# Kernel optimization log

Measured on AMD Instinct MI355X. Metric: run time of the kernel, lower is better.

The kernel has to match this reference:

```python
import jax, jax.numpy as jnp
import numpy as np

BN_EPS = 1e-5

def _conv2d(x, w, b, stride, padding, groups=1):
    out = jax.lax.conv_general_dilated(
        x, w, (stride, stride), padding,
        feature_group_count=groups,
        dimension_numbers=('NCHW', 'OIHW', 'NCHW'))
    return out + b[None, :, None, None]

def _bn(x, g, be, m, v):
    # eval-mode BatchNorm2d
    scale = g / jnp.sqrt(v + BN_EPS)
    return (x - m[None, :, None, None]) * scale[None, :, None, None] + be[None, :, None, None]

def _gelu(x):
    return jax.nn.gelu(x, approximate=False)  # torch nn.GELU default = exact erf

def _forward(x, conv0_w, conv0_b, bn0_g, bn0_b, bn0_m, bn0_v,
             dw_w, dw_b, bn1_g, bn1_b, bn1_m, bn1_v,
             pw_w, pw_b, bn2_g, bn2_b, bn2_m, bn2_v,
             lstm_w, lstm_b, fc_w, fc_b):
    B = x.shape[0]
    nh = conv0_w.shape[0]
    # stem: 4x4 stride-4 conv + BN + GELU -> [B, nh, 8, L]
    y = _gelu(_bn(_conv2d(x, conv0_w, conv0_b, 4, 'VALID'),
                  bn0_g, bn0_b, bn0_m, bn0_v))
    D = dw_w.shape[0]
    for i in range(D):  # MicroBlocks: residual depthwise 3x3 then pointwise 1x1
        r = _gelu(_bn(_conv2d(y, dw_w[i][:, None], dw_b[i], 1, [(1, 1), (1, 1)], groups=nh),
                      bn1_g[i], bn1_b[i], bn1_m[i], bn1_v[i]))
        y = y + r
        y = _gelu(_bn(_conv2d(y, pw_w[i][:, :, None, None], pw_b[i], 1, 'VALID'),
                      bn2_g[i], bn2_b[i], bn2_m[i], bn2_v[i]))
    # ConvLSTM: channel dim nh is the time axis; state is [B, F=8, L]
    L = y.shape[3]
    F = lstm_w.shape[0] // 4
    seq = jnp.transpose(y, (1, 0, 2, 3))  # [nh, B, 8, L]
    h0 = jnp.zeros((B, F, L), y.dtype)

    def step(carry, xt):
        h, c = carry
        comb = jnp.concatenate([xt, h], axis=1)  # [B, 16, L]
        # kernel-size-1 Conv1d == per-position matmul
        A = jnp.einsum('oc,bcl->bol', lstm_w, comb) + lstm_b[None, :, None]
        ai, af, ao, ag = jnp.split(A, 4, axis=1)
        nc = jax.nn.sigmoid(af) * c + jax.nn.sigmoid(ai) * jnp.tanh(ag)
        nhd = jax.nn.sigmoid(ao) * jnp.tanh(nc)
        return (nhd, nc), nhd

    _, ys = jax.lax.scan(step, (h0, h0), seq)  # ys: [nh, B, 8, L]
    feat = jnp.transpose(ys, (1, 0, 2, 3)).reshape(B, nh * F, L)
    # adaptive_avg_pool1d to output size L (== input length) is identity;
    # dropout in eval mode is identity.
    logits = jnp.einsum('bcl,nc->bln', feat, fc_w) + fc_b  # [B, L, nclass]
    return logits

def setup_inputs():
    B, W, NH, D, NCLS, F = 32, 1024, 256, 4, 6625, 8
    key = jax.random.key(0)
    ks = jax.random.split(key, 24)
    n = lambda i, shape, s=0.05: jax.random.normal(ks[i], shape, jnp.float32) * s
    return {
        'x': jax.random.normal(ks[0], (B, 3, 32, W), jnp.float32),
        'conv0_w': n(1, (NH, 3, 4, 4)), 'conv0_b': n(2, (NH,)),
        'bn0_g': 1.0 + n(3, (NH,)), 'bn0_b': n(4, (NH,)),
        'bn0_m': n(5, (NH,)), 'bn0_v': 0.5 + jax.random.uniform(ks[6], (NH,), jnp.float32),
        'dw_w': n(7, (D, NH, 3, 3)), 'dw_b': n(8, (D, NH)),
        'bn1_g': 1.0 + n(9, (D, NH)), 'bn1_b': n(10, (D, NH)),
        'bn1_m': n(11, (D, NH)), 'bn1_v': 0.5 + jax.random.uniform(ks[12], (D, NH), jnp.float32),
        'pw_w': n(13, (D, NH, NH)), 'pw_b': n(14, (D, NH)),
        'bn2_g': 1.0 + n(15, (D, NH)), 'bn2_b': n(16, (D, NH)),
        'bn2_m': n(17, (D, NH)), 'bn2_v': 0.5 + jax.random.uniform(ks[18], (D, NH), jnp.float32),
        'lstm_w': n(19, (4 * F, 2 * F), 0.1), 'lstm_b': n(20, (4 * F,)),
        'fc_w': n(21, (NCLS, NH * F), 0.02), 'fc_b': n(22, (NCLS,)),
    }

def reference(x, conv0_w, conv0_b, bn0_g, bn0_b, bn0_m, bn0_v,
              dw_w, dw_b, bn1_g, bn1_b, bn1_m, bn1_v,
              pw_w, pw_b, bn2_g, bn2_b, bn2_m, bn2_v,
              lstm_w, lstm_b, fc_w, fc_b):
    return _forward(x, conv0_w, conv0_b, bn0_g, bn0_b, bn0_m, bn0_v,
                    dw_w, dw_b, bn1_g, bn1_b, bn1_m, bn1_v,
                    pw_w, pw_b, bn2_g, bn2_b, bn2_m, bn2_v,
                    lstm_w, lstm_b, fc_w, fc_b)
```

## Files before the change

### kernel.cpp

```cpp
#include <hip/hip_runtime.h>
#include <hip/hip_bf16.h>
#include <stdint.h>

#define BNEPS 1e-5f

typedef __bf16 bf16x8 __attribute__((ext_vector_type(8)));
typedef float f32x4 __attribute__((ext_vector_type(4)));

__device__ __forceinline__ float gelu_f(float x) {
    return 0.5f * x * (1.0f + erff(x * 0.70710678118654752440f));
}
__device__ __forceinline__ float sigmoid_f(float x) {
    return 1.0f / (1.0f + __expf(-x));
}
__device__ __forceinline__ float tanh_f(float x) {
    x = fminf(fmaxf(x, -15.0f), 15.0f);
    const float e = __expf(2.0f * x);
    return (e - 1.0f) / (e + 1.0f);
}
__device__ __forceinline__ void async16(const void* g, void* l) {
    __builtin_amdgcn_global_load_lds(
        (const __attribute__((address_space(1))) void*)g,
        (__attribute__((address_space(3))) void*)l,
        16, 0, 0);
}

__global__ __launch_bounds__(256)
void stem_kernel(const float* __restrict__ x, const float* __restrict__ w,
                 const float* __restrict__ cb,
                 const float* __restrict__ bg, const float* __restrict__ bb,
                 const float* __restrict__ bm, const float* __restrict__ bv,
                 float* __restrict__ y0)
{
    __shared__ float sw[64 * 48];
    const int ho = blockIdx.x, b = blockIdx.y, co0 = blockIdx.z * 64;
    const int wo = threadIdx.x;
    for (int i = threadIdx.x; i < 64 * 48; i += 256) sw[i] = w[co0 * 48 + i];
    float p[48];
    #pragma unroll
    for (int c = 0; c < 3; ++c)
        #pragma unroll
        for (int kh = 0; kh < 4; ++kh) {
            const float4 q = *reinterpret_cast<const float4*>(
                &x[((size_t)(b * 3 + c) * 32 + ho * 4 + kh) * 1024 + wo * 4]);
            p[c * 16 + kh * 4 + 0] = q.x;
            p[c * 16 + kh * 4 + 1] = q.y;
            p[c * 16 + kh * 4 + 2] = q.z;
            p[c * 16 + kh * 4 + 3] = q.w;
        }
    __syncthreads();
    for (int c2 = 0; c2 < 64; ++c2) {
        const int co = co0 + c2;
        const float* wp = &sw[c2 * 48];
        float a0 = 0.f, a1 = 0.f, a2 = 0.f, a3 = 0.f;
        #pragma unroll
        for (int i = 0; i < 12; ++i) {
            const float4 wq = *reinterpret_cast<const float4*>(&wp[i * 4]);
            a0 += wq.x * p[i * 4 + 0];
            a1 += wq.y * p[i * 4 + 1];
            a2 += wq.z * p[i * 4 + 2];
            a3 += wq.w * p[i * 4 + 3];
        }
        const float acc = (a0 + a1) + (a2 + a3) + cb[co];
        const float sc = bg[co] / sqrtf(bv[co] + BNEPS);
        const float val = (acc - bm[co]) * sc + bb[co];
        y0[((size_t)(b * 256 + co) * 8 + ho) * 256 + wo] = gelu_f(val);
    }
}

__global__ __launch_bounds__(256)
void dw_kernel(const float* __restrict__ y0, const float* __restrict__ dww,
               const float* __restrict__ dwb,
               const float* __restrict__ bg, const float* __restrict__ bb,
               const float* __restrict__ bm, const float* __restrict__ bv,
               __hip_bfloat16* __restrict__ y1)
{
    __shared__ float tile[8][258];
    const int c = blockIdx.x, b = blockIdx.y, t = threadIdx.x;
    const float* src = &y0[(size_t)(b * 256 + c) * 2048];
    #pragma unroll
    for (int r = 0; r < 8; ++r) tile[r][1 + t] = src[r * 256 + t];
    if (t < 8) { tile[t][0] = 0.f; tile[t][257] = 0.f; }
    float w9[9];
    #pragma unroll
    for (int i = 0; i < 9; ++i) w9[i] = dww[c * 9 + i];
    const float bias = dwb[c];
    const float sc = bg[c] / sqrtf(bv[c] + BNEPS);
    const float sb = bb[c] - bm[c] * sc;
    __syncthreads();
    __hip_bfloat16* dst = &y1[(size_t)(b * 256 + c) * 2048];
    #pragma unroll
    for (int r = 0; r < 8; ++r) {
        float acc = bias;
        #pragma unroll
        for (int kh = 0; kh < 3; ++kh) {
            const int rr = r + kh - 1;
            if (rr < 0 || rr > 7) continue;
            acc += w9[kh * 3 + 0] * tile[rr][t] + w9[kh * 3 + 1] * tile[rr][t + 1]
                 + w9[kh * 3 + 2] * tile[rr][t + 2];
        }
        const float val = gelu_f(acc * sc + sb);
        dst[r * 256 + t] = __float2bfloat16(tile[r][t + 1] + val);
    }
}

__global__ __launch_bounds__(256)
void tr_kernel(const __hip_bfloat16* __restrict__ y1, __hip_bfloat16* __restrict__ y1t)
{
    __shared__ __hip_bfloat16 tile[64][65];
    const int hw0 = blockIdx.x * 64, c0 = blockIdx.y * 64, b = blockIdx.z;
    const int tx = threadIdx.x & 63, ty = threadIdx.x >> 6;
    const __hip_bfloat16* src = &y1[((size_t)b * 256 + c0) * 2048 + hw0];
    #pragma unroll
    for (int r = ty; r < 64; r += 4) tile[r][tx] = src[(size_t)r * 2048 + tx];
    __syncthreads();
    __hip_bfloat16* dst = &y1t[((size_t)b * 2048 + hw0) * 256 + c0];
    #pragma unroll
    for (int r = ty; r < 64; r += 4) dst[(size_t)r * 256 + tx] = tile[tx][r];
}

template<int EPI>
__global__ __launch_bounds__(256)
void gemm_kernel(const __hip_bfloat16* __restrict__ A,
                 const __hip_bfloat16* __restrict__ Bt,
                 float* __restrict__ out, int K, int NT,
                 const float* __restrict__ q0, const float* __restrict__ q1,
                 const float* __restrict__ q2, const float* __restrict__ q3,
                 const float* __restrict__ q4)
{
    __shared__ __hip_bfloat16 sA[2][4096];
    __shared__ __hip_bfloat16 sB[2][4096];
    const int tid = threadIdx.x;
    const int wave = tid >> 6, lane = tid & 63;
    const int m0 = blockIdx.y * 128, n0 = blockIdx.x * 128;

    auto stage = [&](int buf, int kt) {
        const int k0 = kt << 5;
        #pragma unroll
        for (int r = 0; r < 2; ++r) {
            const int e = wave * 1024 + r * 512 + lane * 8;
            const int row = e >> 5, ko = e & 31;
            async16(&A[(size_t)(m0 + row) * K + k0 + ko], &sA[buf][wave * 1024 + r * 512]);
            async16(&Bt[(size_t)(n0 + row) * K + k0 + ko], &sB[buf][wave * 1024 + r * 512]);
        }
    };

    f32x4 acc[4][4];
    #pragma unroll
    for (int i = 0; i < 4; ++i)
        #pragma unroll
        for (int j = 0; j < 4; ++j) acc[i][j] = (f32x4){0.f, 0.f, 0.f, 0.f};

    stage(0, 0);
    const int wm = wave >> 1, wn = wave & 1;
    const int lrow = lane & 15, lgrp = lane >> 4;
    int cur = 0;
    for (int kt = 0; kt < NT; ++kt) {
        __syncthreads();
        if (kt + 1 < NT) stage(cur ^ 1, kt + 1);
        bf16x8 av[4], bw[4];
        #pragma unroll
        for (int i = 0; i < 4; ++i) {
            av[i] = *reinterpret_cast<const bf16x8*>(&sA[cur][(wm * 64 + i * 16 + lrow) * 32 + lgrp * 8]);
            bw[i] = *reinterpret_cast<const bf16x8*>(&sB[cur][(wn * 64 + i * 16 + lrow) * 32 + lgrp * 8]);
        }
        #pragma unroll
        for (int mi = 0; mi < 4; ++mi)
            #pragma unroll
            for (int ni = 0; ni < 4; ++ni)
                acc[mi][ni] = __builtin_amdgcn_mfma_f32_16x16x32_bf16(av[mi], bw[ni], acc[mi][ni], 0, 0, 0);
        cur ^= 1;
    }

    #pragma unroll
    for (int mi = 0; mi < 4; ++mi) {
        const int rowb = m0 + wm * 64 + mi * 16 + lgrp * 4;
        #pragma unroll
        for (int ni = 0; ni < 4; ++ni) {
            const int col = n0 + wn * 64 + ni * 16 + lrow;
            #pragma unroll
            for (int r = 0; r < 4; ++r) {
                const float v = acc[mi][ni][r];
                if (EPI == 0) {
                    const int co = rowb + r;
                    const float sc = q1[co] / sqrtf(q4[co] + BNEPS);
                    const float sb = q2[co] - q3[co] * sc;
                    const float val = gelu_f((v + q0[co]) * sc + sb);
                    const int b_ = col >> 11, hw = col & 2047;
                    out[((size_t)b_ * 256 + co) * 2048 + hw] = val;
                } else {
                    if (col < 6625)
                        out[(size_t)(rowb + r) * 6625 + col] = v + q0[col];
                }
            }
        }
    }
}

__global__ __launch_bounds__(256)
void lstm_kernel(const float* __restrict__ y, const float* __restrict__ lw,
                 const float* __restrict__ lb, __hip_bfloat16* __restrict__ Am)
{
    const int gid = blockIdx.x * 256 + threadIdx.x;
    const int f = gid & 7, pos = gid >> 3;
    const int l = pos & 255, b = pos >> 8;
    float W[4][16], bias[4];
    #pragma unroll
    for (int g = 0; g < 4; ++g) {
        #pragma unroll
        for (int j = 0; j < 16; ++j) W[g][j] = lw[(g * 8 + f) * 16 + j];
        bias[g] = lb[g * 8 + f];
    }
    float h = 0.f, c = 0.f;
    const float* xb = y + (size_t)b * 524288 + f * 256 + l;
    __hip_bfloat16* ob = Am + (size_t)pos * 2048 + f;
    float xn = xb[0];
    for (int t = 0; t < 256; ++t) {
        const float xt = xn;
        if (t < 255) xn = xb[(size_t)(t + 1) * 2048];
        float A0 = bias[0], A1 = bias[1], A2 = bias[2], A3 = bias[3];
        #pragma unroll
        for (int j = 0; j < 8; ++j) {
            const float xj = __shfl(xt, j, 8);
            const float hj = __shfl(h, j, 8);
            A0 += W[0][j] * xj + W[0][8 + j] * hj;
            A1 += W[1][j] * xj + W[1][8 + j] * hj;
            A2 += W[2][j] * xj + W[2][8 + j] * hj;
            A3 += W[3][j] * xj + W[3][8 + j] * hj;
        }
        c = sigmoid_f(A1) * c + sigmoid_f(A0) * tanh_f(A3);
        h = sigmoid_f(A2) * tanh_f(c);
        ob[t * 8] = __float2bfloat16(h);
    }
}

__global__ void cvt_pww_kernel(const float* __restrict__ w, __hip_bfloat16* __restrict__ o, int n)
{
    const int i = blockIdx.x * 256 + threadIdx.x;
    if (i < n) o[i] = __float2bfloat16(w[i]);
}
__global__ void cvt_fcw_kernel(const float* __restrict__ w, __hip_bfloat16* __restrict__ o)
{
    const size_t i = (size_t)blockIdx.x * 256 + threadIdx.x;
    const size_t nrow = i >> 11, k = i & 2047;
    o[i] = (nrow < 6625) ? __float2bfloat16(w[nrow * 2048 + k]) : __float2bfloat16(0.0f);
}

extern "C" void kernel_launch(void* const* d_in, const int* in_sizes, int n_in,
                              void* d_out, int out_size, void* d_ws, size_t ws_size,
                              hipStream_t stream)
{
    const float* x       = (const float*)d_in[0];
    const float* conv0_w = (const float*)d_in[1];
    const float* conv0_b = (const float*)d_in[2];
    const float* bn0_g   = (const float*)d_in[3];
    const float* bn0_b   = (const float*)d_in[4];
    const float* bn0_m   = (const float*)d_in[5];
    const float* bn0_v   = (const float*)d_in[6];
    const float* dw_w    = (const float*)d_in[7];
    const float* dw_b    = (const float*)d_in[8];
    const float* bn1_g   = (const float*)d_in[9];
    const float* bn1_b   = (const float*)d_in[10];
    const float* bn1_m   = (const float*)d_in[11];
    const float* bn1_v   = (const float*)d_in[12];
    const float* pw_w    = (const float*)d_in[13];
    const float* pw_b    = (const float*)d_in[14];
    const float* bn2_g   = (const float*)d_in[15];
    const float* bn2_b   = (const float*)d_in[16];
    const float* bn2_m   = (const float*)d_in[17];
    const float* bn2_v   = (const float*)d_in[18];
    const float* lstm_w  = (const float*)d_in[19];
    const float* lstm_b  = (const float*)d_in[20];
    const float* fc_w    = (const float*)d_in[21];
    const float* fc_b    = (const float*)d_in[22];

    char* ws = (char*)d_ws;
    float* y0            = (float*)(ws);
    __hip_bfloat16* y1   = (__hip_bfloat16*)(ws + 67108864);
    __hip_bfloat16* y1t  = (__hip_bfloat16*)(ws + 100663296);
    __hip_bfloat16* fcwb = (__hip_bfloat16*)(ws + 134217728);
    __hip_bfloat16* pwwb = (__hip_bfloat16*)(ws + 161480704);
    __hip_bfloat16* Am   = (__hip_bfloat16*)(ws + 67108864);

    stem_kernel<<<dim3(8, 32, 4), 256, 0, stream>>>(
        x, conv0_w, conv0_b, bn0_g, bn0_b, bn0_m, bn0_v, y0);
    cvt_pww_kernel<<<1024, 256, 0, stream>>>(pw_w, pwwb, 262144);
    cvt_fcw_kernel<<<53248, 256, 0, stream>>>(fc_w, fcwb);

    for (int i = 0; i < 4; ++i) {
        dw_kernel<<<dim3(256, 32), 256, 0, stream>>>(
            y0, dw_w + i * 2304, dw_b + i * 256,
            bn1_g + i * 256, bn1_b + i * 256, bn1_m + i * 256, bn1_v + i * 256, y1);
        tr_kernel<<<dim3(32, 4, 32), 256, 0, stream>>>(y1, y1t);
        gemm_kernel<0><<<dim3(512, 2), 256, 0, stream>>>(
            pwwb + i * 65536, y1t, y0, 256, 8,
            pw_b + i * 256, bn2_g + i * 256, bn2_b + i * 256, bn2_m + i * 256, bn2_v + i * 256);
    }

    lstm_kernel<<<256, 256, 0, stream>>>(y0, lstm_w, lstm_b, Am);

    gemm_kernel<1><<<dim3(52, 64), 256, 0, stream>>>(
        Am, fcwb, (float*)d_out, 2048, 64,
        fc_b, nullptr, nullptr, nullptr, nullptr);
}
```

Baseline: 767.6 us.

## Specialize FC GEMM with 256x256 tiles, triple buffering, LDS swizzle, block swizzle

After: 710.9 us. -7.4%, faster.

```diff
diff --git a/kernel.cpp b/kernel.cpp
--- a/kernel.cpp
+++ b/kernel.cpp
@@ -119,14 +119,13 @@
     for (int r = ty; r < 64; r += 4) dst[(size_t)r * 256 + tx] = tile[tx][r];
 }
 
-template<int EPI>
 __global__ __launch_bounds__(256)
-void gemm_kernel(const __hip_bfloat16* __restrict__ A,
-                 const __hip_bfloat16* __restrict__ Bt,
-                 float* __restrict__ out, int K, int NT,
-                 const float* __restrict__ q0, const float* __restrict__ q1,
-                 const float* __restrict__ q2, const float* __restrict__ q3,
-                 const float* __restrict__ q4)
+void gemm_pw_kernel(const __hip_bfloat16* __restrict__ A,
+                    const __hip_bfloat16* __restrict__ Bt,
+                    float* __restrict__ out, int K, int NT,
+                    const float* __restrict__ q0, const float* __restrict__ q1,
+                    const float* __restrict__ q2, const float* __restrict__ q3,
+                    const float* __restrict__ q4)
 {
     __shared__ __hip_bfloat16 sA[2][4096];
     __shared__ __hip_bfloat16 sB[2][4096];
@@ -181,17 +180,117 @@
             #pragma unroll
             for (int r = 0; r < 4; ++r) {
                 const float v = acc[mi][ni][r];
-                if (EPI == 0) {
-                    const int co = rowb + r;
-                    const float sc = q1[co] / sqrtf(q4[co] + BNEPS);
-                    const float sb = q2[co] - q3[co] * sc;
-                    const float val = gelu_f((v + q0[co]) * sc + sb);
-                    const int b_ = col >> 11, hw = col & 2047;
-                    out[((size_t)b_ * 256 + co) * 2048 + hw] = val;
-                } else {
-                    if (col < 6625)
-                        out[(size_t)(rowb + r) * 6625 + col] = v + q0[col];
-                }
+                const int co = rowb + r;
+                const float sc = q1[co] / sqrtf(q4[co] + BNEPS);
+                const float sb = q2[co] - q3[co] * sc;
+                const float val = gelu_f((v + q0[co]) * sc + sb);
+                const int b_ = col >> 11, hw = col & 2047;
+                out[((size_t)b_ * 256 + co) * 2048 + hw] = val;
+            }
+        }
+    }
+}
+
+__global__ __launch_bounds__(512, 2)
+void gemm_fc_kernel(const __hip_bfloat16* __restrict__ A,
+                    const __hip_bfloat16* __restrict__ Bt,
+                    const float* __restrict__ fcb,
+                    float* __restrict__ out)
+{
+    constexpr int K = 2048, NT = 64, NTILE = 26;
+    __shared__ __hip_bfloat16 smem[49152];
+    const int tid = threadIdx.x, wave = tid >> 6, lane = tid & 63;
+    const int wm = wave >> 2, wn = wave & 3;
+    const int r = lane & 15, g = lane >> 4;
+    const int swzk = (g ^ ((r >> 1) & 3)) * 8;
+
+    const int bid = blockIdx.x;
+    const int swz = (bid & 7) * 104 + (bid >> 3);
+    const int m0 = (swz / NTILE) * 256;
+    const int n0 = (swz % NTILE) * 256;
+
+    auto stageA = [&](int buf, int kt) {
+        #pragma unroll
+        for (int r2 = 0; r2 < 2; ++r2) {
+            const int e = wave * 128 + r2 * 64 + lane;
+            const int row = e >> 2, slot = e & 3;
+            const int kg = slot ^ ((row >> 1) & 3);
+            async16(&A[(size_t)(m0 + row) * K + kt * 32 + kg * 8],
+                    &smem[buf * 8192 + wave * 1024 + r2 * 512]);
+        }
+    };
+    auto stageB = [&](int buf, int kt) {
+        #pragma unroll
+        for (int r2 = 0; r2 < 2; ++r2) {
+            const int e = wave * 128 + r2 * 64 + lane;
+            const int row = e >> 2, slot = e & 3;
+            const int kg = slot ^ ((row >> 1) & 3);
+            async16(&Bt[(size_t)(n0 + row) * K + kt * 32 + kg * 8],
+                    &smem[24576 + buf * 8192 + wave * 1024 + r2 * 512]);
+        }
+    };
+
+    f32x4 acc[8][4];
+    #pragma unroll
+    for (int i = 0; i < 8; ++i)
+        #pragma unroll
+        for (int j = 0; j < 4; ++j) acc[i][j] = (f32x4){0.f, 0.f, 0.f, 0.f};
+
+    stageA(0, 0); stageB(0, 0);
+    stageA(1, 1); stageB(1, 1);
+
+    int bc = 0;
+    for (int kt = 0; kt < NT; ++kt) {
+        if (kt < NT - 1) asm volatile("s_waitcnt vmcnt(4)" ::: "memory");
+        else             asm volatile("s_waitcnt vmcnt(0)" ::: "memory");
+        asm volatile("s_barrier" ::: "memory");
+
+        const int bn = (bc + 2 >= 3) ? bc - 1 : bc + 2;
+        if (kt + 2 < NT) stageA(bn, kt + 2);
+
+        const __hip_bfloat16* pA = &smem[bc * 8192];
+        const __hip_bfloat16* pB = &smem[24576 + bc * 8192];
+        bf16x8 av[8];
+        #pragma unroll
+        for (int mi = 0; mi < 8; ++mi)
+            av[mi] = *reinterpret_cast<const bf16x8*>(&pA[(wm * 128 + mi * 16 + r) * 32 + swzk]);
+        bf16x8 b0 = *reinterpret_cast<const bf16x8*>(&pB[(wn * 64 + 0 * 16 + r) * 32 + swzk]);
+        bf16x8 b1 = *reinterpret_cast<const bf16x8*>(&pB[(wn * 64 + 1 * 16 + r) * 32 + swzk]);
+
+        __builtin_amdgcn_s_setprio(1);
+        #pragma unroll
+        for (int mi = 0; mi < 8; ++mi) {
+            acc[mi][0] = __builtin_amdgcn_mfma_f32_16x16x32_bf16(av[mi], b0, acc[mi][0], 0, 0, 0);
+            acc[mi][1] = __builtin_amdgcn_mfma_f32_16x16x32_bf16(av[mi], b1, acc[mi][1], 0, 0, 0);
+        }
+        __builtin_amdgcn_s_setprio(0);
+
+        if (kt + 2 < NT) stageB(bn, kt + 2);
+        bf16x8 b2 = *reinterpret_cast<const bf16x8*>(&pB[(wn * 64 + 2 * 16 + r) * 32 + swzk]);
+        bf16x8 b3 = *reinterpret_cast<const bf16x8*>(&pB[(wn * 64 + 3 * 16 + r) * 32 + swzk]);
+
+        __builtin_amdgcn_s_setprio(1);
+        #pragma unroll
+        for (int mi = 0; mi < 8; ++mi) {
+            acc[mi][2] = __builtin_amdgcn_mfma_f32_16x16x32_bf16(av[mi], b2, acc[mi][2], 0, 0, 0);
+            acc[mi][3] = __builtin_amdgcn_mfma_f32_16x16x32_bf16(av[mi], b3, acc[mi][3], 0, 0, 0);
+        }
+        __builtin_amdgcn_s_setprio(0);
+
+        bc = (bc == 2) ? 0 : bc + 1;
+    }
+
+    #pragma unroll
+    for (int mi = 0; mi < 8; ++mi) {
+        const int rowb = m0 + wm * 128 + mi * 16 + g * 4;
+        #pragma unroll
+        for (int ni = 0; ni < 4; ++ni) {
+            const int col = n0 + wn * 64 + ni * 16 + r;
+            if (col < 6625) {
+                const float bb = fcb[col];
+                #pragma unroll
+                for (int rr = 0; rr < 4; ++rr)
+                    out[(size_t)(rowb + rr) * 6625 + col] = acc[mi][ni][rr] + bb;
             }
         }
     }
@@ -292,14 +391,12 @@
             y0, dw_w + i * 2304, dw_b + i * 256,
             bn1_g + i * 256, bn1_b + i * 256, bn1_m + i * 256, bn1_v + i * 256, y1);
         tr_kernel<<<dim3(32, 4, 32), 256, 0, stream>>>(y1, y1t);
-        gemm_kernel<0><<<dim3(512, 2), 256, 0, stream>>>(
+        gemm_pw_kernel<<<dim3(512, 2), 256, 0, stream>>>(
             pwwb + i * 65536, y1t, y0, 256, 8,
             pw_b + i * 256, bn2_g + i * 256, bn2_b + i * 256, bn2_m + i * 256, bn2_v + i * 256);
     }
 
     lstm_kernel<<<256, 256, 0, stream>>>(y0, lstm_w, lstm_b, Am);
 
-    gemm_kernel<1><<<dim3(52, 64), 256, 0, stream>>>(
-        Am, fcwb, (float*)d_out, 2048, 64,
-        fc_b, nullptr, nullptr, nullptr, nullptr);
-}
+    gemm_fc_kernel<<<832, 512, 0, stream>>>(Am, fcwb, fc_b, (float*)d_out);
+}
```
